# Optimization experiments

Hardware: AMD Instinct MI355X
Metric: run time of the kernel (lower is better)

The kernel has to match this reference:

```python
import jax, jax.numpy as jnp
import numpy as np

BN_EPS = 1e-5
GRID = 8  # 8x8 region grid
AU_NUM = 12


def conv2d(x, w, b, stride=1, pad=0):
    # x: [B,C,H,W], w: [O,I,kh,kw]
    y = jax.lax.conv_general_dilated(
        x, w, (stride, stride), [(pad, pad), (pad, pad)],
        dimension_numbers=("NCHW", "OIHW", "NCHW"))
    return y + b[None, :, None, None]


def bn_eval(x, gamma, beta, mean, var):
    inv = jax.lax.rsqrt(var + BN_EPS)
    return (x - mean[None, :, None, None]) * (gamma * inv)[None, :, None, None] + beta[None, :, None, None]


def region_layer(x, gamma, beta, mean, var, cw, cb):
    # x: [B,C,H,W]; per-network params indexed by k = i*j + j (faithful to source)
    B, C, H, W = x.shape
    ph, pw = H // GRID, W // GRID
    # -> [64, B, C, ph, pw]
    p = x.reshape(B, C, GRID, ph, GRID, pw).transpose(2, 4, 0, 1, 3, 5).reshape(GRID * GRID, B, C, ph, pw)
    ii = jnp.arange(GRID)[:, None]
    jj = jnp.arange(GRID)[None, :]
    idx = (ii * jj + jj).reshape(-1)  # replicates self.networks[i*j+j]

    def per_patch(xp, g, bt, m, v, w, b):
        xn = bn_eval(xp, g, bt, m, v)
        xr = jax.nn.relu(xn)
        return conv2d(xr, w, b, stride=1, pad=1) + xp

    out = jax.vmap(per_patch)(p, gamma[idx], beta[idx], mean[idx], var[idx], cw[idx], cb[idx])
    # [64,B,C,ph,pw] -> [B,C,H,W]
    return out.reshape(GRID, GRID, B, C, ph, pw).transpose(2, 3, 0, 4, 1, 5).reshape(B, C, H, W)


def maxpool2(x):
    return jax.lax.reduce_window(x, -jnp.inf, jax.lax.max, (1, 1, 2, 2), (1, 1, 2, 2), "VALID")


def setup_inputs() -> dict:
    key = jax.random.key(0)
    ks = iter(jax.random.split(key, 40))
    n = lambda shape, s=0.05: jax.random.normal(next(ks), shape, jnp.float32) * s
    d = {}
    d["x"] = jax.random.normal(next(ks), (32, 3, 170, 170), jnp.float32)
    d["conv1_w"] = n((32, 3, 11, 11)); d["conv1_b"] = n((32,))
    NG = GRID * GRID
    d["rl_gamma"] = 1.0 + n((NG, 32)); d["rl_beta"] = n((NG, 32))
    d["rl_mean"] = n((NG, 32)); d["rl_var"] = 0.5 + jax.random.uniform(next(ks), (NG, 32), jnp.float32)
    d["rl_cw"] = n((NG, 32, 32, 3, 3)); d["rl_cb"] = n((NG, 32))
    d["bn_gamma"] = 1.0 + n((32,)); d["bn_beta"] = n((32,))
    d["bn_mean"] = n((32,)); d["bn_var"] = 0.5 + jax.random.uniform(next(ks), (32,), jnp.float32)
    d["conv2_w"] = n((16, 32, 8, 8)); d["conv2_b"] = n((16,))
    d["conv3_w"] = n((16, 16, 8, 8)); d["conv3_b"] = n((16,))
    d["conv4_w"] = n((16, 16, 6, 6)); d["conv4_b"] = n((16,))
    d["conv5_w"] = n((16, 16, 5, 5)); d["conv5_b"] = n((16,))
    d["fc1_w"] = n((4096, 16 * 27 * 27), 0.01); d["fc1_b"] = n((4096,))
    d["fc2_w"] = n((2048, 4096), 0.01); d["fc2_b"] = n((2048,))
    d["fc3_w"] = n((AU_NUM * 2, 2048), 0.01); d["fc3_b"] = n((AU_NUM * 2,))
    return d


def reference(x, conv1_w, conv1_b, rl_gamma, rl_beta, rl_mean, rl_var, rl_cw, rl_cb,
              bn_gamma, bn_beta, bn_mean, bn_var, conv2_w, conv2_b, conv3_w, conv3_b,
              conv4_w, conv4_b, conv5_w, conv5_b, fc1_w, fc1_b, fc2_w, fc2_b, fc3_w, fc3_b):
    B = x.shape[0]
    h = conv2d(x, conv1_w, conv1_b)                       # [B,32,160,160]
    h = region_layer(h, rl_gamma, rl_beta, rl_mean, rl_var, rl_cw, rl_cb)
    h = jax.nn.relu(h)
    h = maxpool2(h)                                       # [B,32,80,80]
    h = bn_eval(h, bn_gamma, bn_beta, bn_mean, bn_var)
    h = jax.nn.relu(conv2d(h, conv2_w, conv2_b))          # [B,16,73,73]
    h = jax.nn.relu(conv2d(h, conv3_w, conv3_b))          # [B,16,66,66]
    h = jax.nn.relu(conv2d(h, conv4_w, conv4_b, stride=2))  # [B,16,31,31]
    h = jax.nn.relu(conv2d(h, conv5_w, conv5_b))          # [B,16,27,27]
    h = h.reshape(B, -1)
    h = jax.nn.relu(h @ fc1_w.T + fc1_b)
    h = jax.nn.relu(h @ fc2_w.T + fc2_b)  # dropout = identity (eval)
    h = h @ fc3_w.T + fc3_b
    h = h.reshape(B, 2, AU_NUM)
    return jax.nn.log_softmax(h, axis=1)
```

## Files before the change

kernel.cpp:

```cpp
#include <hip/hip_runtime.h>
#include <hip/hip_bf16.h>

typedef __hip_bfloat16 bf16;
typedef __attribute__((ext_vector_type(8))) short short8;
typedef __attribute__((ext_vector_type(4))) float f32x4;
typedef __attribute__((ext_vector_type(16))) float f32x16;

__device__ __forceinline__ float b2f(const bf16 v){ return __bfloat162float(v); }
__device__ __forceinline__ float ld(const float* p, long i){ return p[i]; }
__device__ __forceinline__ float ld(const bf16*  p, long i){ return b2f(p[i]); }

__device__ __forceinline__ unsigned f2bf_u(float f){
    union { float f; unsigned u; } a; a.f = f;
    unsigned r = a.u + 0x7FFFu + ((a.u >> 16) & 1u);
    return r >> 16;
}

__device__ __forceinline__ short8 pack8(const float* v){
    union { __hip_bfloat162 h[4]; short8 s; } r;
    #pragma unroll
    for (int i=0;i<4;i++)
        r.h[i] = __float22bfloat162_rn(float2{v[2*i], v[2*i+1]});
    return r.s;
}

__device__ __forceinline__ uint2 pack4(const float* v){
    union { __hip_bfloat162 h[2]; uint2 u; } r;
    r.h[0] = __float22bfloat162_rn(float2{v[0], v[1]});
    r.h[1] = __float22bfloat162_rn(float2{v[2], v[3]});
    return r.u;
}

__device__ __forceinline__ void unp8(uint4 u, float* v){
    union { unsigned x; float f; } a;
    a.x = u.x<<16; v[0]=a.f; a.x = u.x&0xffff0000u; v[1]=a.f;
    a.x = u.y<<16; v[2]=a.f; a.x = u.y&0xffff0000u; v[3]=a.f;
    a.x = u.z<<16; v[4]=a.f; a.x = u.z&0xffff0000u; v[5]=a.f;
    a.x = u.w<<16; v[6]=a.f; a.x = u.w&0xffff0000u; v[7]=a.f;
}

__device__ __forceinline__ void unp4(uint2 u, float* v){
    union { unsigned x; float f; } a;
    a.x = u.x<<16; v[0]=a.f; a.x = u.x&0xffff0000u; v[1]=a.f;
    a.x = u.y<<16; v[2]=a.f; a.x = u.y&0xffff0000u; v[3]=a.f;
}

#define GLD_LDS16(g, l) __builtin_amdgcn_global_load_lds( \
    (const __attribute__((address_space(1))) void*)(g), \
    (__attribute__((address_space(3))) void*)(l), 16, 0, 0)

#define OFF_C1W   0
#define OFF_C1B   11616
#define OFF_RLG   11648
#define OFF_RLB   13696
#define OFF_RLM   15744
#define OFF_RLV   17792
#define OFF_RLCW  19840
#define OFF_RLCB  609664
#define OFF_BNG   611712
#define OFF_BNB   611744
#define OFF_BNM   611776
#define OFF_BNV   611808
#define OFF_C2W   611840
#define OFF_C2B   644608
#define OFF_C3W   644624
#define OFF_C3B   661008
#define OFF_C4W   661024
#define OFF_C4B   670240
#define OFF_C5W   670256
#define OFF_C5B   676656
#define OFF_F1B   676672
#define OFF_F2B   680768
#define OFF_F3B   682816
#define P_TOTAL   682840
#define OFF_WB2   P_TOTAL
#define OFF_WB3   (P_TOTAL + 16384)
#define OFF_WC1   (P_TOTAL + 16384 + 8192)
#define P_END     (OFF_WC1 + 8448)

#define SZ_RL  589824
#define SZ_WB2 32768
#define SZ_WB3 16384
#define SZ_WC1 16896

__global__ void k_sniff(const void* __restrict__ x, int* __restrict__ flag)
{
    const bf16* xb = (const bf16*)x;
    const float v = fabsf(b2f(xb[2*threadIdx.x]));
    const int ok = (v >= 1e-6f && v <= 1e6f) ? 1 : 0;
    __shared__ int cnt;
    if (threadIdx.x == 0) cnt = 0;
    __syncthreads();
    atomicAdd(&cnt, ok);
    __syncthreads();
    if (threadIdx.x == 0) *flag = (cnt >= 192) ? 0 : 1;
}

struct CvtArgs { const void* src[23]; int off[23]; const void* cw; const void* w2; const void* w3; int total; };

__device__ __forceinline__ float getv(const void* p, long i, bool isf){
    return isf ? ((const float*)p)[i] : b2f(((const bf16*)p)[i]);
}

__global__ __launch_bounds__(256) void k_cvt(CvtArgs a, const int* __restrict__ flag,
                                             float* __restrict__ P)
{
    const bool isf = (*flag != 0);
    const int i1 = a.total;
    const int i2 = i1 + SZ_RL;
    const int i3 = i2 + SZ_WB2;
    const int i4 = i3 + SZ_WB3;
    const int i5 = i4 + SZ_WC1;
    for (int idx = blockIdx.x*256 + threadIdx.x; idx < i5; idx += gridDim.x*256){
        if (idx < i1){
            if (idx >= OFF_RLCW && idx < OFF_RLCB) continue;
            int k = 0;
            #pragma unroll
            for (int j = 1; j < 23; j++) if (idx >= a.off[j]) k = j;
            P[idx] = getv(a.src[k], idx - a.off[k], isf);
        } else if (idx < i2){
            const int d = idx - i1;
            const int net = d / 9216, dn = d % 9216;
            const int tap = dn >> 10, rem = dn & 1023;
            const int half = rem >> 9, lane = (rem >> 3) & 63, j = rem & 7;
            const int co = half*16 + (lane & 15);
            const int ci = ((lane >> 4) << 3) + j;
            const long sidx = (long)((net*32 + co)*32 + ci)*9 + tap;
            ((unsigned short*)(P + OFF_RLCW))[d] = (unsigned short)f2bf_u(getv(a.cw, sidx, isf));
        } else if (idx < i3){
            const int d = idx - i2;
            const int j = d & 7, lane = (d >> 3) & 63, tap = d >> 9;
            const int n = lane & 15, k = ((lane >> 4) << 3) + j;
            const int ci = k, ky = tap >> 3, kx = tap & 7;
            const long sidx = (long)((n*32 + ci)*8 + ky)*8 + kx;
            ((unsigned short*)(P + OFF_WB2))[d] = (unsigned short)f2bf_u(getv(a.w2, sidx, isf));
        } else if (idx < i4){
            const int d = idx - i3;
            const int j = d & 7, lane = (d >> 3) & 63, pair = d >> 9;
            const int n = lane & 15, k = ((lane >> 4) << 3) + j;
            const int tsel = k >> 4, ci = k & 15;
            const int ky = pair >> 2, kx = ((pair & 3) << 1) + tsel;
            const long sidx = (long)((n*16 + ci)*8 + ky)*8 + kx;
            ((unsigned short*)(P + OFF_WB3))[d] = (unsigned short)f2bf_u(getv(a.w3, sidx, isf));
        } else {
            const int d = idx - i4;
            const int ky = d / 1536, rem = d % 1536;
            const int ch = rem >> 9, rem2 = rem & 511;
            const int lane = rem2 >> 3, j = rem2 & 7;
            const int co = lane & 31, h5 = lane >> 5;
            const int kx = ch*4 + h5*2 + (j >> 2), ci = j & 3;
            float v = 0.f;
            if (ci < 3 && kx < 11)
                v = getv(a.src[0], (long)((co*3 + ci)*11 + ky)*11 + kx, isf);
            ((unsigned short*)(P + OFF_WC1))[d] = (unsigned short)f2bf_u(v);
        }
    }
}

__global__ __launch_bounds__(256,3) void k_conv1M(const void* __restrict__ x,
        const int* __restrict__ flag, const float* __restrict__ P, unsigned short* __restrict__ out)
{
    __shared__ unsigned short xs[18*44*4];
    __shared__ unsigned short wsm[SZ_WC1];
    const int t = threadIdx.x;
    const int y0 = blockIdx.x*8, x0 = blockIdx.y*32, b = blockIdx.z;
    { const uint4* src = (const uint4*)(P + OFF_WC1);
      uint4* dst = (uint4*)wsm;
      for (int e=t; e<2112; e+=256) dst[e] = src[e]; }
    const bool isf = (*flag) != 0;
    for (int e=t; e<792; e+=256){
        const int r = e/44, c = e%44;
        const long base = ((long)(b*3)*170 + (y0+r))*170 + min(x0+c, 169);
        float v0, v1, v2;
        if (isf){
            const float* xf = (const float*)x;
            v0 = xf[base]; v1 = xf[base+28900]; v2 = xf[base+57800];
        } else {
            const bf16* xf = (const bf16*)x;
            v0 = b2f(xf[base]); v1 = b2f(xf[base+28900]); v2 = b2f(xf[base+57800]);
        }
        uint2 u;
        u.x = f2bf_u(v0) | (f2bf_u(v1) << 16);
        u.y = f2bf_u(v2);
        *(uint2*)&xs[(r*44+c)*4] = u;
    }
    __syncthreads();
    const int wave = t>>6, lane = t&63;
    const int n = lane & 31, h5 = lane >> 5;
    const int r0 = wave*2;
    f32x16 acc0 = {0.f}, acc1 = {0.f};
    #pragma unroll
    for (int e=0;e<16;e++){ acc0[e]=0.f; acc1[e]=0.f; }
    #pragma unroll 1
    for (int ky=0; ky<11; ky++){
        #pragma unroll
        for (int ch=0; ch<3; ch++){
            const short8 aw = *(const short8*)&wsm[((ky*3+ch)*64 + lane)*8];
            const int kx0 = ch*4 + h5*2;
            const int a0 = ((r0+ky)*44 + n + kx0)*4;
            const int a1 = ((r0+1+ky)*44 + n + kx0)*4;
            union { uint2 u2[2]; short8 s; } ub0, ub1;
            ub0.u2[0] = *(const uint2*)&xs[a0];
            ub0.u2[1] = *(const uint2*)&xs[a0+4];
            ub1.u2[0] = *(const uint2*)&xs[a1];
            ub1.u2[1] = *(const uint2*)&xs[a1+4];
            acc0 = __builtin_amdgcn_mfma_f32_32x32x16_bf16(aw, ub0.s, acc0, 0,0,0);
            acc1 = __builtin_amdgcn_mfma_f32_32x32x16_bf16(aw, ub1.s, acc1, 0,0,0);
        }
    }
    unsigned short* opb = out + ((long)b*25600 + (long)(y0+r0)*160 + x0 + n)*32;
    #pragma unroll
    for (int g=0; g<4; g++){
        const int co0 = 8*g + 4*h5;
        const f32x4 bv = *(const f32x4*)&P[OFF_C1B + co0];
        float s0[4], s1[4];
        #pragma unroll
        for (int r=0;r<4;r++){ s0[r] = acc0[4*g+r] + bv[r]; s1[r] = acc1[4*g+r] + bv[r]; }
        *(uint2*)(opb + co0) = pack4(s0);
        *(uint2*)(opb + 160*32 + co0) = pack4(s1);
    }
}

__global__ __launch_bounds__(256,2) void k_regionM(const unsigned short* __restrict__ in,
        const float* __restrict__ P, unsigned short* __restrict__ pooled)
{
    __shared__ unsigned short s_in[484*32];
    __shared__ unsigned short wsm[9216];
    __shared__ float sc[32], sh[32];
    const int t = threadIdx.x;
    const int b = blockIdx.x & 31, kk = blockIdx.x >> 5;
    const int gi = kk >> 3, gj = kk & 7;
    const int net = gj*(gi+1);
    const long pbase = ((long)b*25600 + (long)(gi*20)*160 + gj*20)*32;
    if (t < 32){
        const float inv = rsqrtf(P[OFF_RLV+net*32+t]+1e-5f)*P[OFF_RLG+net*32+t];
        sc[t] = inv; sh[t] = P[OFF_RLB+net*32+t] - P[OFF_RLM+net*32+t]*inv;
    }
    { const uint4* src = (const uint4*)((const unsigned short*)(P+OFF_RLCW) + (size_t)net*9216);
      uint4* dst = (uint4*)wsm;
      for (int e=t; e<1152; e+=256) dst[e] = src[e]; }
    __syncthreads();
    for (int e=t; e<1936; e+=256){
        const int o = e & 3, p = e >> 2;
        const int pr = p/22, pc = p%22;
        short8 pk = {0,0,0,0,0,0,0,0};
        if (pr>0 && pr<21 && pc>0 && pc<21){
            const long a = pbase + ((long)(pr-1)*160 + (pc-1))*32 + o*8;
            const uint4 u = *(const uint4*)&in[a];
            float v[8];
            unp8(u, v);
            #pragma unroll
            for (int j=0;j<8;j++){
                const int ci = o*8 + j;
                v[j] = fmaxf(fmaf(v[j], sc[ci], sh[ci]), 0.f);
            }
            pk = pack8(v);
        }
        *(short8*)&s_in[p*32 + o*8] = pk;
    }
    __syncthreads();
    const int wave = t>>6, lane = t&63;
    const int q = lane>>4, n = lane&15;
    const int dr = n>>2, dc = n&3;
    const int nt = (wave==0) ? 7 : 6;
    int trs[7], tcs[7];
    #pragma unroll
    for (int i=0;i<7;i++){ const int tt = 4*i + wave; trs[i] = tt/5; tcs[i] = tt - 5*(tt/5); }
    f32x4 acc[7][2];
    {   float bias_v[2][4];
        #pragma unroll
        for (int h=0;h<2;h++)
            #pragma unroll
            for (int r=0;r<4;r++) bias_v[h][r] = P[OFF_RLCB + net*32 + h*16 + q*4 + r];
        #pragma unroll
        for (int i=0;i<7;i++)
            #pragma unroll
            for (int h=0;h<2;h++)
                acc[i][h] = (f32x4){bias_v[h][0], bias_v[h][1], bias_v[h][2], bias_v[h][3]};
    }
    #pragma unroll 1
    for (int tap=0; tap<9; tap++){
        const int ky = tap/3, kx = tap - 3*(tap/3);
        const short8 a0 = *(const short8*)&wsm[(tap*2+0)*512 + lane*8];
        const short8 a1 = *(const short8*)&wsm[(tap*2+1)*512 + lane*8];
        #pragma unroll
        for (int i=0;i<7;i++){
            if (i < nt){
                const int srow = trs[i]*4 + dr + ky, scol = tcs[i]*4 + dc + kx;
                const short8 bx = *(const short8*)&s_in[(srow*22 + scol)*32 + q*8];
                acc[i][0] = __builtin_amdgcn_mfma_f32_16x16x32_bf16(a0, bx, acc[i][0], 0,0,0);
                acc[i][1] = __builtin_amdgcn_mfma_f32_16x16x32_bf16(a1, bx, acc[i][1], 0,0,0);
            }
        }
    }
    float bnsc[2][4], bnsh[2][4];
    #pragma unroll
    for (int h=0;h<2;h++)
        #pragma unroll
        for (int r=0;r<4;r++){
            const int co = h*16 + q*4 + r;
            const float inv = rsqrtf(P[OFF_BNV+co]+1e-5f)*P[OFF_BNG+co];
            bnsc[h][r] = inv; bnsh[h][r] = P[OFF_BNB+co] - P[OFF_BNM+co]*inv;
        }
    const bool wr = ((n & 5) == 0);
    #pragma unroll
    for (int i=0;i<7;i++){
        if (i < nt){
            const int prow = trs[i]*4 + dr, pcol = tcs[i]*4 + dc;
            const long ra = pbase + ((long)prow*160 + pcol)*32;
            const long pa0 = ((long)b*6400 + (long)(gi*10 + trs[i]*2 + (dr>>1))*80
                              + gj*10 + tcs[i]*2 + (dc>>1))*32;
            #pragma unroll
            for (int h=0;h<2;h++){
                const uint2 ru = *(const uint2*)&in[ra + h*16 + q*4];
                float res[4];
                unp4(ru, res);
                float pv[4];
                #pragma unroll
                for (int r=0;r<4;r++){
                    float v = acc[i][h][r] + res[r];
                    v = fmaxf(v, 0.f);
                    v = fmaxf(v, __shfl_xor(v, 1, 64));
                    v = fmaxf(v, __shfl_xor(v, 4, 64));
                    pv[r] = fmaf(v, bnsc[h][r], bnsh[h][r]);
                }
                if (wr) *(uint2*)&pooled[pa0 + h*16 + q*4] = pack4(pv);
            }
        }
    }
}

template<int CIN, int HIN, int WIN, int HOUT, int WOUT, bool NHWC_OUT>
__global__ __launch_bounds__(256) void k_convM(const unsigned short* __restrict__ in,
        const unsigned short* __restrict__ WB, const float* __restrict__ bias,
        void* __restrict__ outv)
{
    constexpr int PP = 23;
    constexpr bool C32 = (CIN == 32);
    __shared__ unsigned short xs[PP*PP*CIN];
    __shared__ unsigned short ws[C32 ? 16*64*8 : 32*64*8];
    const int t = threadIdx.x;
    const int col0 = blockIdx.x*16, row0 = blockIdx.y*16, b = blockIdx.z;
    for (int e = t; e < PP*PP*(CIN/8); e += 256){
        const int o = e % (CIN/8), pix = e / (CIN/8);
        int rr = row0 + pix/PP; if (rr > HIN-1) rr = HIN-1;
        int cc = col0 + pix%PP; if (cc > WIN-1) cc = WIN-1;
        const uint4 v = *(const uint4*)&in[((long)b*HIN*WIN + (long)rr*WIN + cc)*CIN + o*8];
        *(uint4*)&xs[pix*CIN + o*8] = v;
    }
    const int wave = t>>6, lane = t&63;
    const int quad = lane>>4, n16 = lane&15;
    const float bv = bias[n16];
    f32x4 acc[4];
    #pragma unroll
    for (int mt=0;mt<4;mt++) acc[mt] = (f32x4){bv,bv,bv,bv};
    if constexpr (C32){
        for (int ch=0; ch<4; ch++){
            __syncthreads();
            const unsigned* src = (const unsigned*)WB + ch*4096;
            for (int e=t; e<4096; e+=256) ((unsigned*)ws)[e] = src[e];
            __syncthreads();
            #pragma unroll 1
            for (int tap=0; tap<16; tap++){
                const int tg = ch*16+tap, ky = tg>>3, kx = tg&7;
                const short8 bw = *(const short8*)&ws[(tap*64+lane)*8];
                #pragma unroll
                for (int mt=0; mt<4; mt++){
                    const int pr = wave*4+mt+ky, pc = n16+kx;
                    const short8 av = *(const short8*)&xs[(pr*PP+pc)*32 + quad*8];
                    acc[mt] = __builtin_amdgcn_mfma_f32_16x16x32_bf16(av, bw, acc[mt], 0,0,0);
                }
            }
        }
    } else {
        for (int e=t; e<8192; e+=256) ((unsigned*)ws)[e] = ((const unsigned*)WB)[e];
        __syncthreads();
        #pragma unroll 1
        for (int pair=0; pair<32; pair++){
            const int ky = pair>>2, kx0 = (pair&3)*2;
            const short8 bw = *(const short8*)&ws[(pair*64+lane)*8];
            #pragma unroll
            for (int mt=0; mt<4; mt++){
                const int pr = wave*4+mt+ky, pc = n16 + kx0 + (quad>>1);
                const short8 av = *(const short8*)&xs[(pr*PP+pc)*16 + (quad&1)*8];
                acc[mt] = __builtin_amdgcn_mfma_f32_16x16x32_bf16(av, bw, acc[mt], 0,0,0);
            }
        }
    }
    #pragma unroll
    for (int mt=0; mt<4; mt++){
        const int orow = row0 + wave*4 + mt;
        if (orow >= HOUT) continue;
        const int ocol = col0 + quad*4;
        #pragma unroll
        for (int r=0;r<4;r++){
            if (ocol + r < WOUT){
                const float v = fmaxf(acc[mt][r], 0.f);
                if constexpr (NHWC_OUT)
                    ((unsigned short*)outv)[((long)b*HOUT*WOUT + (long)orow*WOUT + ocol + r)*16 + n16]
                        = (unsigned short)f2bf_u(v);
                else
                    ((float*)outv)[((long)(b*16 + n16)*HOUT + orow)*WOUT + ocol + r] = v;
            }
        }
    }
}

template<int CIN, int COUT, int KS, int STRIDE, int HIN, int WIN, int HOUT, int WOUT,
         int NG, int OW, bool BF16OUT, int ROWPAD>
__global__ __launch_bounds__(256,2) void k_convN(const float* __restrict__ in,
        const float* __restrict__ w, const float* __restrict__ bias, void* __restrict__ outv)
{
    __shared__ float wl[CIN*KS*KS];
    const int co = blockIdx.y, b = blockIdx.z;
    for (int j=threadIdx.x; j<CIN*KS*KS; j+=blockDim.x) wl[j] = w[co*CIN*KS*KS + j];
    __syncthreads();
    const int i = blockIdx.x*blockDim.x + threadIdx.x;
    if (i >= HOUT*NG) return;
    const int y = i / NG, x0 = (i % NG) * OW;
    float acc[OW];
    const float bv = bias[co];
    #pragma unroll
    for (int j=0;j<OW;j++) acc[j]=bv;
    constexpr int SPAN = STRIDE*(OW-1) + KS;
    for (int ci=0; ci<CIN; ci++){
        #pragma unroll
        for (int ky=0; ky<KS; ky++){
            const float* ip = in + ((long)(b*CIN+ci)*HIN + (STRIDE*y+ky))*WIN + STRIDE*x0;
            float v[SPAN];
            #pragma unroll
            for (int j=0;j<SPAN;j++) v[j]=ip[j];
            const float* wr = &wl[(ci*KS+ky)*KS];
            #pragma unroll
            for (int kx=0;kx<KS;kx++){
                const float wv = wr[kx];
                #pragma unroll
                for (int j=0;j<OW;j++) acc[j] = fmaf(v[STRIDE*j+kx], wv, acc[j]);
            }
        }
    }
    if constexpr (BF16OUT){
        unsigned short* op = (unsigned short*)outv + (long)b*ROWPAD + (co*HOUT + y)*WOUT + x0;
        #pragma unroll
        for (int j=0;j<OW;j++)
            if (x0 + j < WOUT) op[j] = (unsigned short)f2bf_u(fmaxf(acc[j], 0.f));
    } else {
        float* op = (float*)outv + ((long)(b*COUT+co)*HOUT + y)*WOUT + x0;
        #pragma unroll
        for (int j=0;j<OW;j++)
            if (x0 + j < WOUT) op[j] = fmaxf(acc[j], 0.f);
    }
}

__global__ void k_binit(float* __restrict__ y, const float* __restrict__ bias, int N)
{
    const int i = blockIdx.x*256 + threadIdx.x;
    if (i < 32*N) y[i] = bias[i % N];
}

__global__ void k_fc1prep(float* __restrict__ y, const float* __restrict__ bias,
                          unsigned short* __restrict__ xp)
{
    const int i = blockIdx.x*256 + threadIdx.x;
    if (i < 32*4096) y[i] = bias[i & 4095];
    if (i < 19968){
        const int r = i / 624;
        xp[(long)r*12288 + 11664 + (i - r*624)] = 0;
    }
}

__global__ __launch_bounds__(256) void k_xpack(const float* __restrict__ in,
        unsigned short* __restrict__ out, int rows, int Ksrc, int Kdst, int relu)
{
    const int per = Kdst >> 3;
    const int i = blockIdx.x*256 + threadIdx.x;
    if (i >= rows*per) return;
    const int row = i / per, k = (i - row*per)*8;
    float v[8];
    if (k + 8 <= Ksrc){
        *(f32x4*)&v[0] = *(const f32x4*)&in[(long)row*Ksrc + k];
        *(f32x4*)&v[4] = *(const f32x4*)&in[(long)row*Ksrc + k + 4];
    } else {
        #pragma unroll
        for (int j=0;j<8;j++) v[j] = (k + j < Ksrc) ? in[(long)row*Ksrc + k + j] : 0.f;
    }
    if (relu){
        #pragma unroll
        for (int j=0;j<8;j++) v[j] = fmaxf(v[j], 0.f);
    }
    *(short8*)&out[(long)row*Kdst + k] = pack8(v);
}

template<typename WT>
__device__ __forceinline__ void fcl_body(const unsigned short* __restrict__ x,
        const WT* __restrict__ w, float* __restrict__ y,
        int Kw, int Khat, int N, int Kc, int Nvalid, unsigned char* lbuf)
{
    constexpr bool WF = __is_same(WT, float);
    const int t = threadIdx.x;
    const int wave = t>>6, lane = t&63;
    const int quad = lane>>4, n16 = lane&15;
    const int og = wave>>1, bh = wave&1;
    const int bx = blockIdx.x;
    const int start = blockIdx.y*Kc;
    int steps = 0;
    {   const int rem = Kw - start;
        const int sa = Kc >> 7;
        if (rem > 0){ steps = (rem + 127) >> 7; if (steps > sa) steps = sa; }
    }
    f32x4 acc = {0.f,0.f,0.f,0.f};
    const unsigned short* xp = x + (long)(bh*16 + n16)*Khat;
    const int row = og*16 + n16;

    auto stage = [&](int s, int bsel){
        const int k0 = start + (s<<7);
        const bool swz = (k0 + 128 <= Kw);
        unsigned char* base = lbuf + bsel*16384;
        if constexpr (WF){
            const int r0 = wave*8;
            #pragma unroll
            for (int c=0;c<4;c++){
                const int rr = r0 + 2*c + (lane>>5);
                const int cs = swz ? ((lane&31) ^ (rr&7)) : (lane&31);
                long koff = (long)k0 + cs*4;
                const float* ga = w + (long)(bx*32 + rr)*Kw + koff;
                if (!swz && (koff + 4 > Kw)) ga = w + (long)(bx*32 + rr)*Kw;
                GLD_LDS16(ga, base + (r0 + 2*c)*512);
            }
        } else {
            const int r0 = wave*8;
            #pragma unroll
            for (int c=0;c<2;c++){
                const int rr = r0 + 4*c + (lane>>4);
                const int cs = swz ? ((lane&15) ^ (rr&7)) : (lane&15);
                long koff = (long)k0 + cs*8;
                const WT* ga = w + (long)(bx*32 + rr)*Kw + koff;
                if (!swz && (koff + 8 > Kw)) ga = w + (long)(bx*32 + rr)*Kw;
                GLD_LDS16(ga, base + (r0 + 4*c)*256);
            }
        }
    };
    auto consume = [&](int s, int bsel){
        const int k0 = start + (s<<7);
        const bool swz = (k0 + 128 <= Kw);
        const unsigned char* base = lbuf + bsel*16384;
        #pragma unroll
        for (int kk=0; kk<4; kk++){
            const int ka = k0 + kk*32 + quad*8;
            const short8 x8 = *(const short8*)&xp[ka];
            short8 bw;
            if constexpr (WF){
                const int c0 = kk*8 + quad*2;
                const int p0 = swz ? (c0 ^ (row&7)) : c0;
                const int p1 = swz ? ((c0+1) ^ (row&7)) : (c0+1);
                float wv[8];
                *(f32x4*)&wv[0] = *(const f32x4*)&base[row*512 + p0*16];
                *(f32x4*)&wv[4] = *(const f32x4*)&base[row*512 + p1*16];
                bw = pack8(wv);
            } else {
                const int c0 = kk*4 + quad;
                const int p0 = swz ? (c0 ^ (row&7)) : c0;
                bw = *(const short8*)&base[row*256 + p0*16];
            }
            acc = __builtin_amdgcn_mfma_f32_16x16x32_bf16(x8, bw, acc, 0,0,0);
        }
    };

    if (steps > 0){
        stage(0, 0);
        __syncthreads();
        for (int s=0; s<steps; s++){
            if (s+1 < steps) stage(s+1, (s+1)&1);
            consume(s, s&1);
            __syncthreads();
        }
    }
    const int o = bx*32 + og*16 + n16;
    if (o < Nvalid){
        #pragma unroll
        for (int r=0;r<4;r++)
            atomicAdd(&y[(long)(bh*16 + quad*4 + r)*N + o], acc[r]);
    }
}

__global__ __launch_bounds__(256) void k_fcL(const unsigned short* __restrict__ x,
        const void* __restrict__ w, const int* __restrict__ flag,
        float* __restrict__ y, int Kw, int Khat, int N, int Kc, int Nvalid)
{
    __shared__ unsigned char lbuf[2*16384];
    if (*flag) fcl_body<float>(x, (const float*)w, y, Kw, Khat, N, Kc, Nvalid, lbuf);
    else       fcl_body<bf16 >(x, (const bf16 *)w, y, Kw, Khat, N, Kc, Nvalid, lbuf);
}

template<typename WT>
__device__ __forceinline__ void fcm_loop(const unsigned short* __restrict__ xp,
        const WT* __restrict__ wp, int start, int end, int quad, f32x4& acc)
{
    const int nfull = (end - start) >> 5;
    const int end32 = start + (nfull << 5);
    const int qo = quad*8;

    short8 xA, xB, xC;
    short8 bwA, bwB, bwC;
    f32x4 wA0, wA1, wB0, wB1, wC0, wC1;

    auto loadA = [&](int k0){
        const int ka = k0 + qo;
        xA = *(const short8*)&xp[ka];
        if constexpr (__is_same(WT, bf16)) bwA = *(const short8*)&wp[ka];
        else { wA0 = *(const f32x4*)&wp[ka]; wA1 = *(const f32x4*)&wp[ka+4]; }
    };
    auto loadB = [&](int k0){
        const int ka = k0 + qo;
        xB = *(const short8*)&xp[ka];
        if constexpr (__is_same(WT, bf16)) bwB = *(const short8*)&wp[ka];
        else { wB0 = *(const f32x4*)&wp[ka]; wB1 = *(const f32x4*)&wp[ka+4]; }
    };
    auto loadC = [&](int k0){
        const int ka = k0 + qo;
        xC = *(const short8*)&xp[ka];
        if constexpr (__is_same(WT, bf16)) bwC = *(const short8*)&wp[ka];
        else { wC0 = *(const f32x4*)&wp[ka]; wC1 = *(const f32x4*)&wp[ka+4]; }
    };
    auto compA = [&](){
        short8 bw;
        if constexpr (__is_same(WT, bf16)) bw = bwA;
        else { float wv[8]; *(f32x4*)&wv[0]=wA0; *(f32x4*)&wv[4]=wA1; bw = pack8(wv); }
        acc = __builtin_amdgcn_mfma_f32_16x16x32_bf16(xA, bw, acc, 0,0,0);
    };
    auto compB = [&](){
        short8 bw;
        if constexpr (__is_same(WT, bf16)) bw = bwB;
        else { float wv[8]; *(f32x4*)&wv[0]=wB0; *(f32x4*)&wv[4]=wB1; bw = pack8(wv); }
        acc = __builtin_amdgcn_mfma_f32_16x16x32_bf16(xB, bw, acc, 0,0,0);
    };
    auto compC = [&](){
        short8 bw;
        if constexpr (__is_same(WT, bf16)) bw = bwC;
        else { float wv[8]; *(f32x4*)&wv[0]=wC0; *(f32x4*)&wv[4]=wC1; bw = pack8(wv); }
        acc = __builtin_amdgcn_mfma_f32_16x16x32_bf16(xC, bw, acc, 0,0,0);
    };

    if (nfull >= 3){
        loadA(start); loadB(start+32); loadC(start+64);
        int j = 0;
        for (; j + 6 <= nfull; j += 3){
            compA(); loadA(start + ((j+3)<<5));
            compB(); loadB(start + ((j+4)<<5));
            compC(); loadC(start + ((j+5)<<5));
        }
        const int rem = nfull - j;
        if (rem == 3){ compA(); compB(); compC(); }
        else if (rem == 4){
            compA(); loadA(start + ((j+3)<<5));
            compB(); compC(); compA();
        } else {
            compA(); loadA(start + ((j+3)<<5));
            compB(); loadB(start + ((j+4)<<5));
            compC(); compA(); compB();
        }
    } else if (nfull == 2){
        loadA(start); loadB(start+32); compA(); compB();
    } else if (nfull == 1){
        loadA(start); compA();
    }
    if (end32 < end){
        const int ka = end32 + qo;
        float xv[8], wv[8];
        #pragma unroll
        for (int j=0;j<8;j++){
            const bool v = (ka + j) < end;
            xv[j] = v ? b2f(((const bf16*)xp)[ka+j]) : 0.f;
            wv[j] = v ? (float)ld(wp, ka+j) : 0.f;
        }
        acc = __builtin_amdgcn_mfma_f32_16x16x32_bf16(pack8(xv), pack8(wv), acc, 0,0,0);
    }
}

__global__ __launch_bounds__(256,4) void k_fcM(const unsigned short* __restrict__ x,
        const void* __restrict__ w, const int* __restrict__ flag,
        float* __restrict__ y, int K, int N, int Kc, int Nvalid)
{
    const int t = threadIdx.x;
    const int wave = t>>6, lane = t&63;
    const int quad = lane>>4, n16 = lane&15;
    const int og = wave>>1, bh = wave&1;
    const int o = blockIdx.x*32 + og*16 + n16;
    const int orow = (o < Nvalid) ? o : (Nvalid-1);
    const int xrow = bh*16 + n16;
    const int start = blockIdx.y*Kc;
    const int end = min(K, start + Kc);
    f32x4 acc = {0.f,0.f,0.f,0.f};
    const unsigned short* xp = x + (long)xrow*K;
    if (*flag) fcm_loop<float>(xp, (const float*)w + (long)orow*K, start, end, quad, acc);
    else       fcm_loop<bf16 >(xp, (const bf16 *)w + (long)orow*K, start, end, quad, acc);
    if (o < Nvalid){
        #pragma unroll
        for (int r=0;r<4;r++)
            atomicAdd(&y[(long)(bh*16 + quad*4 + r)*N + o], acc[r]);
    }
}

__global__ void k_lsm(const float* __restrict__ in, const int* __restrict__ flag,
                      void* __restrict__ out)
{
    const int i = threadIdx.x;
    if (i >= 384) return;
    const int b = i/12, au = i%12;
    const float a0 = in[b*24+au], a1 = in[b*24+12+au];
    const float m = fmaxf(a0,a1);
    const float lse = m + logf(expf(a0-m)+expf(a1-m));
    const float o0 = a0-lse, o1 = a1-lse;
    if (*flag){
        ((float*)out)[b*24+au]    = o0;
        ((float*)out)[b*24+12+au] = o1;
    } else {
        ((bf16*)out)[b*24+au]    = __float2bfloat16(o0);
        ((bf16*)out)[b*24+12+au] = __float2bfloat16(o1);
    }
}

extern "C" void kernel_launch(void* const* d_in, const int* in_sizes, int n_in,
                              void* d_out, int out_size, void* d_ws, size_t ws_size,
                              hipStream_t stream) {
    (void)in_sizes; (void)n_in; (void)out_size; (void)ws_size;
    const void* x = d_in[0];

    float* A = (float*)d_ws;
    float* B = A + 26214400;
    float* P = B + 6553600;
    int* flag = (int*)(P + P_END);
    unsigned short* Xp = (unsigned short*)(P + P_END + 16);
    unsigned short* Abf = (unsigned short*)A;
    unsigned short* Bbf = (unsigned short*)B;

    CvtArgs a;
    const int src_idx[23] = {1,2,3,4,5,6,7,8,9,10,11,12,13,14,15,16,17,18,19,20,22,24,26};
    const int offs[23] = {OFF_C1W,OFF_C1B,OFF_RLG,OFF_RLB,OFF_RLM,OFF_RLV,OFF_RLCW,OFF_RLCB,
                          OFF_BNG,OFF_BNB,OFF_BNM,OFF_BNV,OFF_C2W,OFF_C2B,OFF_C3W,OFF_C3B,
                          OFF_C4W,OFF_C4B,OFF_C5W,OFF_C5B,OFF_F1B,OFF_F2B,OFF_F3B};
    for (int j=0;j<23;j++){ a.src[j] = d_in[src_idx[j]]; a.off[j] = offs[j]; }
    a.cw = d_in[7]; a.w2 = d_in[13]; a.w3 = d_in[15];
    a.total = P_TOTAL;

    k_sniff<<<1,256,0,stream>>>(x, flag);
    k_cvt<<<(P_TOTAL+SZ_RL+SZ_WB2+SZ_WB3+SZ_WC1+255)/256,256,0,stream>>>(a, flag, P);
    k_conv1M<<<dim3(20,5,32),256,0,stream>>>(x, flag, P, Abf);
    k_regionM<<<2048,256,0,stream>>>(Abf, P, Bbf);
    k_convM<32,80,80,73,73,true><<<dim3(5,5,32),256,0,stream>>>(Bbf, (const unsigned short*)(P+OFF_WB2), P+OFF_C2B, (void*)Abf);
    k_convM<16,73,73,66,66,false><<<dim3(5,5,32),256,0,stream>>>(Abf, (const unsigned short*)(P+OFF_WB3), P+OFF_C3B, (void*)B);
    k_convN<16,16,6,2,66,66,31,31,8,4,false,0><<<dim3(1,16,32),256,0,stream>>>(B, P+OFF_C4W, P+OFF_C4B, A);
    k_convN<16,16,5,1,31,31,27,27,7,4,true,12288><<<dim3(1,16,32),256,0,stream>>>(A, P+OFF_C5W, P+OFF_C5B, Xp);
    k_fc1prep<<<512,256,0,stream>>>(A, P+OFF_F1B, Xp);
    k_fcL<<<dim3(128,16),256,0,stream>>>(Xp, d_in[21], flag, A, 11664, 12288, 4096, 768, 4096);
    k_xpack<<<(32*(4096/8)+255)/256,256,0,stream>>>(A, Xp, 32, 4096, 4096, 1);
    k_binit<<<(32*2048+255)/256,256,0,stream>>>(B, P+OFF_F2B, 2048);
    k_fcL<<<dim3(64,16),256,0,stream>>>(Xp, d_in[23], flag, B, 4096, 4096, 2048, 256, 2048);
    k_xpack<<<(32*(2048/8)+255)/256,256,0,stream>>>(B, Xp, 32, 2048, 2048, 1);
    k_binit<<<(32*24+255)/256,256,0,stream>>>(A, P+OFF_F3B, 24);
    k_fcM<<<dim3(1,64),256,0,stream>>>(Xp, d_in[25], flag, A, 2048, 24, 32, 24);
    k_lsm<<<1,384,0,stream>>>(A, flag, d_out);
}
```

Baseline: 584.0 us.

## Fuse small setup kernels into neighbours and halve FC split-K

Folds the dtype sniff into the parameter-conversion kernel, so every block computes the flag locally. The FC1 bias init and Xp pad zeroing move into a dedicated conv5 kernel, and each bias init is merged with the following ReLU+bf16 pack. Together these cut the number of launches. The FC layers' split-K factor drops from 16 to 8, with twice the K chunk per block and launch_bounds occupancy 4. This means fewer atomics but less parallelism for each FC layer.

Result: faster. 569.7 us (-2.4%).

```diff
diff --git a/kernel.cpp b/kernel.cpp
--- a/kernel.cpp
+++ b/kernel.cpp
@@ -83,29 +83,28 @@
 #define SZ_WB3 16384
 #define SZ_WC1 16896
 
-__global__ void k_sniff(const void* __restrict__ x, int* __restrict__ flag)
-{
-    const bf16* xb = (const bf16*)x;
-    const float v = fabsf(b2f(xb[2*threadIdx.x]));
-    const int ok = (v >= 1e-6f && v <= 1e6f) ? 1 : 0;
+struct CvtArgs { const void* src[23]; int off[23]; const void* cw; const void* w2; const void* w3;
+                 const void* x0; int total; };
+
+__device__ __forceinline__ float getv(const void* p, long i, bool isf){
+    return isf ? ((const float*)p)[i] : b2f(((const bf16*)p)[i]);
+}
+
+__global__ __launch_bounds__(256) void k_cvt(CvtArgs a, int* __restrict__ flag,
+                                             float* __restrict__ P)
+{
     __shared__ int cnt;
     if (threadIdx.x == 0) cnt = 0;
     __syncthreads();
-    atomicAdd(&cnt, ok);
+    {
+        const bf16* xb = (const bf16*)a.x0;
+        const float v = fabsf(b2f(xb[2*threadIdx.x]));
+        if (v >= 1e-6f && v <= 1e6f) atomicAdd(&cnt, 1);
+    }
     __syncthreads();
-    if (threadIdx.x == 0) *flag = (cnt >= 192) ? 0 : 1;
-}
-
-struct CvtArgs { const void* src[23]; int off[23]; const void* cw; const void* w2; const void* w3; int total; };
-
-__device__ __forceinline__ float getv(const void* p, long i, bool isf){
-    return isf ? ((const float*)p)[i] : b2f(((const bf16*)p)[i]);
-}
-
-__global__ __launch_bounds__(256) void k_cvt(CvtArgs a, const int* __restrict__ flag,
-                                             float* __restrict__ P)
-{
-    const bool isf = (*flag != 0);
+    const bool isf = (cnt < 192);
+    if (blockIdx.x == 0 && threadIdx.x == 0) *flag = isf ? 1 : 0;
+
     const int i1 = a.total;
     const int i2 = i1 + SZ_RL;
     const int i3 = i2 + SZ_WB2;
@@ -280,9 +279,9 @@
     }
     #pragma unroll 1
     for (int tap=0; tap<9; tap++){
-        const int ky = tap/3, kx = tap - 3*(tap/3);
         const short8 a0 = *(const short8*)&wsm[(tap*2+0)*512 + lane*8];
         const short8 a1 = *(const short8*)&wsm[(tap*2+1)*512 + lane*8];
+        const int ky = tap/3, kx = tap - 3*(tap/3);
         #pragma unroll
         for (int i=0;i<7;i++){
             if (i < nt){
@@ -407,9 +406,9 @@
 }
 
 template<int CIN, int COUT, int KS, int STRIDE, int HIN, int WIN, int HOUT, int WOUT,
-         int NG, int OW, bool BF16OUT, int ROWPAD>
+         int NG, int OW>
 __global__ __launch_bounds__(256,2) void k_convN(const float* __restrict__ in,
-        const float* __restrict__ w, const float* __restrict__ bias, void* __restrict__ outv)
+        const float* __restrict__ w, const float* __restrict__ bias, float* __restrict__ out)
 {
     __shared__ float wl[CIN*KS*KS];
     const int co = blockIdx.y, b = blockIdx.z;
@@ -439,56 +438,71 @@
             }
         }
     }
-    if constexpr (BF16OUT){
-        unsigned short* op = (unsigned short*)outv + (long)b*ROWPAD + (co*HOUT + y)*WOUT + x0;
-        #pragma unroll
-        for (int j=0;j<OW;j++)
-            if (x0 + j < WOUT) op[j] = (unsigned short)f2bf_u(fmaxf(acc[j], 0.f));
-    } else {
-        float* op = (float*)outv + ((long)(b*COUT+co)*HOUT + y)*WOUT + x0;
-        #pragma unroll
-        for (int j=0;j<OW;j++)
-            if (x0 + j < WOUT) op[j] = fmaxf(acc[j], 0.f);
-    }
-}
-
-__global__ void k_binit(float* __restrict__ y, const float* __restrict__ bias, int N)
+    float* op = out + ((long)(b*COUT+co)*HOUT + y)*WOUT + x0;
+    #pragma unroll
+    for (int j=0;j<OW;j++)
+        if (x0 + j < WOUT) op[j] = fmaxf(acc[j], 0.f);
+}
+
+__global__ __launch_bounds__(256,2) void k_conv5F(const float* __restrict__ in,
+        const float* __restrict__ P, unsigned short* __restrict__ xp, float* __restrict__ y)
+{
+    __shared__ float wl[16*25];
+    const int co = blockIdx.y, b = blockIdx.z;
+    const int t = threadIdx.x;
+    for (int j=t; j<400; j+=256) wl[j] = P[OFF_C5W + co*400 + j];
+    {   const int lin = (b*16 + co)*256 + t;
+        y[lin] = P[OFF_F1B + (lin & 4095)];
+    }
+    if (co == 0 && t < 208){
+        unsigned short* pp = xp + (long)b*12288 + 11664 + t*3;
+        pp[0] = 0; pp[1] = 0; pp[2] = 0;
+    }
+    __syncthreads();
+    if (t >= 27*7) return;
+    const int yy = t / 7, x0 = (t % 7) * 4;
+    float acc[4];
+    const float bv = P[OFF_C5B + co];
+    #pragma unroll
+    for (int j=0;j<4;j++) acc[j]=bv;
+    for (int ci=0; ci<16; ci++){
+        #pragma unroll
+        for (int ky=0; ky<5; ky++){
+            const float* ip = in + ((long)(b*16+ci)*31 + (yy+ky))*31 + x0;
+            float v[8];
+            #pragma unroll
+            for (int j=0;j<8;j++) v[j]=ip[j];
+            const float* wr = &wl[(ci*5+ky)*5];
+            #pragma unroll
+            for (int kx=0;kx<5;kx++){
+                const float wv = wr[kx];
+                #pragma unroll
+                for (int j=0;j<4;j++) acc[j] = fmaf(v[j+kx], wv, acc[j]);
+            }
+        }
+    }
+    unsigned short* op = xp + (long)b*12288 + (co*27 + yy)*27 + x0;
+    #pragma unroll
+    for (int j=0;j<4;j++)
+        if (x0 + j < 27) op[j] = (unsigned short)f2bf_u(fmaxf(acc[j], 0.f));
+}
+
+__global__ __launch_bounds__(256) void k_pk(const float* __restrict__ in,
+        unsigned short* __restrict__ out, float* __restrict__ y,
+        const float* __restrict__ bias, int N, int ny, int rows, int K)
 {
     const int i = blockIdx.x*256 + threadIdx.x;
-    if (i < 32*N) y[i] = bias[i % N];
-}
-
-__global__ void k_fc1prep(float* __restrict__ y, const float* __restrict__ bias,
-                          unsigned short* __restrict__ xp)
-{
-    const int i = blockIdx.x*256 + threadIdx.x;
-    if (i < 32*4096) y[i] = bias[i & 4095];
-    if (i < 19968){
-        const int r = i / 624;
-        xp[(long)r*12288 + 11664 + (i - r*624)] = 0;
-    }
-}
-
-__global__ __launch_bounds__(256) void k_xpack(const float* __restrict__ in,
-        unsigned short* __restrict__ out, int rows, int Ksrc, int Kdst, int relu)
-{
-    const int per = Kdst >> 3;
-    const int i = blockIdx.x*256 + threadIdx.x;
-    if (i >= rows*per) return;
-    const int row = i / per, k = (i - row*per)*8;
+    if (i < ny){ y[i] = bias[i % N]; return; }
+    const int d = i - ny;
+    const int per = K >> 3;
+    if (d >= rows*per) return;
+    const int row = d / per, k = (d - row*per)*8;
     float v[8];
-    if (k + 8 <= Ksrc){
-        *(f32x4*)&v[0] = *(const f32x4*)&in[(long)row*Ksrc + k];
-        *(f32x4*)&v[4] = *(const f32x4*)&in[(long)row*Ksrc + k + 4];
-    } else {
-        #pragma unroll
-        for (int j=0;j<8;j++) v[j] = (k + j < Ksrc) ? in[(long)row*Ksrc + k + j] : 0.f;
-    }
-    if (relu){
-        #pragma unroll
-        for (int j=0;j<8;j++) v[j] = fmaxf(v[j], 0.f);
-    }
-    *(short8*)&out[(long)row*Kdst + k] = pack8(v);
+    *(f32x4*)&v[0] = *(const f32x4*)&in[(long)row*K + k];
+    *(f32x4*)&v[4] = *(const f32x4*)&in[(long)row*K + k + 4];
+    #pragma unroll
+    for (int j=0;j<8;j++) v[j] = fmaxf(v[j], 0.f);
+    *(short8*)&out[(long)row*K + k] = pack8(v);
 }
 
 template<typename WT>
@@ -583,7 +597,7 @@
     }
 }
 
-__global__ __launch_bounds__(256) void k_fcL(const unsigned short* __restrict__ x,
+__global__ __launch_bounds__(256,4) void k_fcL(const unsigned short* __restrict__ x,
         const void* __restrict__ w, const int* __restrict__ flag,
         float* __restrict__ y, int Kw, int Khat, int N, int Kc, int Nvalid)
 {
@@ -733,6 +747,7 @@
     unsigned short* Xp = (unsigned short*)(P + P_END + 16);
     unsigned short* Abf = (unsigned short*)A;
     unsigned short* Bbf = (unsigned short*)B;
+    float* Bhi = B + 5000000;
 
     CvtArgs a;
     const int src_idx[23] = {1,2,3,4,5,6,7,8,9,10,11,12,13,14,15,16,17,18,19,20,22,24,26};
@@ -741,23 +756,20 @@
                           OFF_C4W,OFF_C4B,OFF_C5W,OFF_C5B,OFF_F1B,OFF_F2B,OFF_F3B};
     for (int j=0;j<23;j++){ a.src[j] = d_in[src_idx[j]]; a.off[j] = offs[j]; }
     a.cw = d_in[7]; a.w2 = d_in[13]; a.w3 = d_in[15];
+    a.x0 = x;
     a.total = P_TOTAL;
 
-    k_sniff<<<1,256,0,stream>>>(x, flag);
     k_cvt<<<(P_TOTAL+SZ_RL+SZ_WB2+SZ_WB3+SZ_WC1+255)/256,256,0,stream>>>(a, flag, P);
     k_conv1M<<<dim3(20,5,32),256,0,stream>>>(x, flag, P, Abf);
     k_regionM<<<2048,256,0,stream>>>(Abf, P, Bbf);
     k_convM<32,80,80,73,73,true><<<dim3(5,5,32),256,0,stream>>>(Bbf, (const unsigned short*)(P+OFF_WB2), P+OFF_C2B, (void*)Abf);
     k_convM<16,73,73,66,66,false><<<dim3(5,5,32),256,0,stream>>>(Abf, (const unsigned short*)(P+OFF_WB3), P+OFF_C3B, (void*)B);
-    k_convN<16,16,6,2,66,66,31,31,8,4,false,0><<<dim3(1,16,32),256,0,stream>>>(B, P+OFF_C4W, P+OFF_C4B, A);
-    k_convN<16,16,5,1,31,31,27,27,7,4,true,12288><<<dim3(1,16,32),256,0,stream>>>(A, P+OFF_C5W, P+OFF_C5B, Xp);
-    k_fc1prep<<<512,256,0,stream>>>(A, P+OFF_F1B, Xp);
-    k_fcL<<<dim3(128,16),256,0,stream>>>(Xp, d_in[21], flag, A, 11664, 12288, 4096, 768, 4096);
-    k_xpack<<<(32*(4096/8)+255)/256,256,0,stream>>>(A, Xp, 32, 4096, 4096, 1);
-    k_binit<<<(32*2048+255)/256,256,0,stream>>>(B, P+OFF_F2B, 2048);
-    k_fcL<<<dim3(64,16),256,0,stream>>>(Xp, d_in[23], flag, B, 4096, 4096, 2048, 256, 2048);
-    k_xpack<<<(32*(2048/8)+255)/256,256,0,stream>>>(B, Xp, 32, 2048, 2048, 1);
-    k_binit<<<(32*24+255)/256,256,0,stream>>>(A, P+OFF_F3B, 24);
+    k_convN<16,16,6,2,66,66,31,31,8,4><<<dim3(1,16,32),256,0,stream>>>(B, P+OFF_C4W, P+OFF_C4B, Bhi);
+    k_conv5F<<<dim3(1,16,32),256,0,stream>>>(Bhi, P, Xp, A);
+    k_fcL<<<dim3(128,8),256,0,stream>>>(Xp, d_in[21], flag, A, 11664, 12288, 4096, 1536, 4096);
+    k_pk<<<(65536+16384+255)/256,256,0,stream>>>(A, Xp, B, P+OFF_F2B, 2048, 65536, 32, 4096);
+    k_fcL<<<dim3(64,8),256,0,stream>>>(Xp, d_in[23], flag, B, 4096, 4096, 2048, 512, 2048);
+    k_pk<<<(768+8192+255)/256,256,0,stream>>>(B, Xp, A, P+OFF_F3B, 24, 768, 32, 2048);
     k_fcM<<<dim3(1,64),256,0,stream>>>(Xp, d_in[25], flag, A, 2048, 24, 32, 24);
     k_lsm<<<1,384,0,stream>>>(A, flag, d_out);
 }
```
